# Optimization experiments

Hardware: AMD Instinct MI355X
Metric: run time of the kernel (lower is better)

## Reference

```python
import jax, jax.numpy as jnp
import numpy as np
from jax import lax


def setup_inputs() -> dict:
    key = jax.random.key(0)
    ks = jax.random.split(key, 5)
    B, Cin, H, W = 16, 256, 64, 64
    E, Cout, K = 8, 256, 3
    fan_in = Cin * K * K
    wscale = 1.0 / np.sqrt(fan_in)
    return {
        "x": jax.random.normal(ks[0], (B, Cin, H, W), dtype=jnp.float32),
        "weight": jax.random.normal(ks[1], (E, Cout, Cin, K, K), dtype=jnp.float32) * wscale,
        "bias": jax.random.normal(ks[2], (E, Cout), dtype=jnp.float32) * wscale,
        "routing_w": jax.random.normal(ks[3], (E, Cin), dtype=jnp.float32) * (1.0 / np.sqrt(Cin)),
        "routing_b": jnp.zeros((E,), dtype=jnp.float32),
    }


def reference(x, weight, bias, routing_w, routing_b):
    # Routing: global avg pool -> linear -> sigmoid  => [B, E]
    pooled = x.mean(axis=(2, 3))                                  # [B, Cin]
    routing = jax.nn.sigmoid(pooled @ routing_w.T + routing_b)    # [B, E]

    # Per-sample aggregated conv weights/bias (mixture of experts)
    agg_w = jnp.einsum('be,eoihw->boihw', routing, weight)        # [B, O, I, kh, kw]
    agg_b = routing @ bias                                        # [B, O]

    # Per-sample conv2d (stride=1, padding=1, dilation=1, groups=1), batched via vmap
    def conv_one(xi, wi):
        return lax.conv_general_dilated(
            xi[None], wi,
            window_strides=(1, 1),
            padding=((1, 1), (1, 1)),
            dimension_numbers=('NCHW', 'OIHW', 'NCHW'),
        )[0]

    out = jax.vmap(conv_one)(x, agg_w)                            # [B, O, H, W]
    return out + agg_b[:, :, None, None]
```

## Files before the change

### kernel.cpp

```cpp
#include <hip/hip_runtime.h>
#include <hip/hip_bf16.h>

typedef unsigned short u16;
typedef __attribute__((ext_vector_type(8))) short bf16x8;
typedef __attribute__((ext_vector_type(8))) short short8;
typedef __attribute__((ext_vector_type(4))) float f32x4;

#define B_ 16
#define CIN 256
#define COUT 256
#define NPIX 4096
#define E_ 8
#define HP 66
#define PPIX (HP*HP)
#define KTOT 2304
#define NKT 36

__device__ __forceinline__ u16 f2bf(float f){
    union { float f; unsigned int u; } v; v.f = f;
    return (u16)((v.u + 0x7FFFu + ((v.u >> 16) & 1u)) >> 16);
}

__device__ __forceinline__ void gload(const u16* g, u16* l){
    __builtin_amdgcn_global_load_lds(
        (const __attribute__((address_space(1))) unsigned int*)g,
        (__attribute__((address_space(3))) unsigned int*)l, 16, 0, 0);
}

__global__ void k_xt(const float* __restrict__ x, u16* __restrict__ xt2,
                     float* __restrict__ pooled){
    __shared__ float tile[64][65];
    int bid = blockIdx.x;
    int t = threadIdx.x;

    if (bid < 520){
        int gid = bid*256 + t;
        int u4 = gid & 31;
        int pl = gid >> 5;
        if (pl < B_*260){
            int bb = pl / 260;
            int pi = pl - bb*260;
            int yy, xx;
            if (pi < 66)      { yy = 0;  xx = pi; }
            else if (pi < 132){ yy = 65; xx = pi - 66; }
            else { int q = pi - 132; yy = 1 + (q >> 1); xx = (q & 1) ? 65 : 0; }
            uint4 z = {0u,0u,0u,0u};
            *(uint4*)(xt2 + ((size_t)bb*PPIX + yy*HP + xx)*CIN + u4*8) = z;
        }
    }

    int b = bid >> 8, ct = (bid >> 6) & 3, pt = bid & 63;
    int c0 = ct*64, p0 = pt*64;
    #pragma unroll
    for (int iter = 0; iter < 4; ++iter){
        int idx = t*4 + iter*1024;
        int r = idx >> 6, c4 = idx & 63;
        float4 v = *(const float4*)(x + ((size_t)(b*CIN + c0 + r))*NPIX + p0 + c4);
        tile[r][c4+0] = v.x; tile[r][c4+1] = v.y; tile[r][c4+2] = v.z; tile[r][c4+3] = v.w;
        float rs = v.x + v.y + v.z + v.w;
        #pragma unroll
        for (int off = 1; off < 16; off <<= 1) rs += __shfl_xor(rs, off, 64);
        if ((t & 15) == 0) atomicAdd(&pooled[b*CIN + c0 + r], rs);
    }
    __syncthreads();
    #pragma unroll
    for (int iter = 0; iter < 2; ++iter){
        int unit = t + iter*256;
        int g_l = unit & 7, pr = unit >> 3;
        unsigned int d0, d1, d2, d3;
        asm("v_cvt_pk_bf16_f32 %0, %1, %2" : "=v"(d0)
            : "v"(tile[g_l*8+0][pr]), "v"(tile[g_l*8+1][pr]));
        asm("v_cvt_pk_bf16_f32 %0, %1, %2" : "=v"(d1)
            : "v"(tile[g_l*8+2][pr]), "v"(tile[g_l*8+3][pr]));
        asm("v_cvt_pk_bf16_f32 %0, %1, %2" : "=v"(d2)
            : "v"(tile[g_l*8+4][pr]), "v"(tile[g_l*8+5][pr]));
        asm("v_cvt_pk_bf16_f32 %0, %1, %2" : "=v"(d3)
            : "v"(tile[g_l*8+6][pr]), "v"(tile[g_l*8+7][pr]));
        uint4 o; o.x = d0; o.y = d1; o.z = d2; o.w = d3;
        int p = p0 + pr;
        int yy = p >> 6, xx = p & 63;
        *(uint4*)(xt2 + ((size_t)b*PPIX + (yy+1)*HP + (xx+1))*CIN + c0 + g_l*8) = o;
    }
}

__global__ __launch_bounds__(576) void k_aggw(
    const float* __restrict__ weight, const float* __restrict__ pooled,
    const float* __restrict__ rw, const float* __restrict__ rb,
    const float* __restrict__ bias,
    u16* __restrict__ aggw, float* __restrict__ aggb)
{
    __shared__ float wls[E_][2304];
    __shared__ float r_s[B_*E_];
    int o = blockIdx.x, t = threadIdx.x;

    if (t < B_*E_){
        int b = t >> 3, e = t & 7;
        const float4* pp = (const float4*)(pooled + b*CIN);
        const float4* wp = (const float4*)(rw + e*CIN);
        float s = 0.f;
        #pragma unroll
        for (int i = 0; i < 64; ++i){
            float4 a = pp[i], c = wp[i];
            s += a.x*c.x + a.y*c.y + a.z*c.z + a.w*c.w;
        }
        s = s * (1.0f/(float)NPIX) + rb[e];
        r_s[t] = 1.0f/(1.0f + __expf(-s));
    }
    #pragma unroll
    for (int e = 0; e < E_; ++e){
        const float4* src = (const float4*)(weight + ((size_t)(e*COUT + o))*2304);
        float4* dst = (float4*)wls[e];
        dst[t] = src[t];
    }
    __syncthreads();

    if (t < B_){
        float s = 0.f;
        #pragma unroll
        for (int e = 0; e < E_; ++e) s += r_s[t*E_+e]*bias[e*COUT+o];
        aggb[t*COUT + o] = s;
    }

    {
        int grp = (t >= 288);
        int u = t - grp*288;
        int tp = u >> 5, cg = u & 31;
        float w[E_][8];
        #pragma unroll
        for (int e = 0; e < E_; ++e)
            #pragma unroll
            for (int j = 0; j < 8; ++j)
                w[e][j] = wls[e][(cg*8 + j)*9 + tp];

        int b0 = grp*8;
        for (int bb = 0; bb < 8; ++bb){
            int b = b0 + bb;
            float acc[8];
            #pragma unroll
            for (int j = 0; j < 8; ++j) acc[j] = 0.f;
            #pragma unroll
            for (int e = 0; e < E_; ++e){
                float r = r_s[b*E_ + e];
                #pragma unroll
                for (int j = 0; j < 8; ++j) acc[j] += r * w[e][j];
            }
            short8 ov;
            #pragma unroll
            for (int jj = 0; jj < 4; ++jj){
                unsigned int d;
                asm("v_cvt_pk_bf16_f32 %0, %1, %2" : "=v"(d) : "v"(acc[2*jj]), "v"(acc[2*jj+1]));
                ov[2*jj]   = (short)(d & 0xFFFF);
                ov[2*jj+1] = (short)(d >> 16);
            }
            *(short8*)(aggw + (((size_t)(b*COUT + o))*9 + tp)*CIN + cg*8) = ov;
        }
    }
}

__global__ __launch_bounds__(512, 2) void k_conv(
    const u16* __restrict__ aggw, const u16* __restrict__ xt2,
    const float* __restrict__ aggb, float* __restrict__ out)
{
    __shared__ __align__(16) u16 lds[65536];

    int orig = blockIdx.x;
    int bid = (orig & 7)*32 + (orig >> 3);

    int b  = bid >> 4;
    int nt = bid & 15;
    int y0 = nt << 2;

    int t = threadIdx.x;
    int lane = t & 63;
    int w = t >> 6;
    int wm = (w >> 2) << 7;
    int wn = (w & 3) << 6;
    int l16 = lane & 15;
    int kh4 = lane >> 4;
    int sw  = l16 & 7;

    int tr = t >> 3;
    int tc = t & 7;
    int sc = tc ^ (tr & 7);

    const u16* aSrc = aggw + (size_t)b*COUT*9*CIN + (size_t)tr*KTOT + sc*8;
    const u16* bSrc = xt2 + ((size_t)b*PPIX + (size_t)y0*HP + tr)*CIN + sc*8;

    f32x4 acc[8][4];
    #pragma unroll
    for (int i = 0; i < 8; ++i)
        #pragma unroll
        for (int j = 0; j < 4; ++j){
            f32x4 z = {0.f,0.f,0.f,0.f};
            acc[i][j] = z;
        }

    auto stage = [&](int kt, int bufn){
        int tap = kt >> 2;
        int c0  = (kt & 3) << 6;
        int kh  = tap / 3, kw = tap - kh*3;
        const u16* a0 = aSrc + tap*CIN + c0;
        const u16* b0 = bSrc + (kh*HP + kw)*CIN + c0;
        u16* dA = lds + bufn*32768 + w*512;
        u16* dB = dA + 16384;
        #pragma unroll
        for (int i = 0; i < 4; ++i)
            gload(a0 + (size_t)i*64*KTOT, dA + i*4096);
        #pragma unroll
        for (int i = 0; i < 4; ++i)
            gload(b0 + (size_t)i*HP*CIN, dB + i*4096);
    };

    int ck0 = ((kh4    ) ^ sw) * 8;
    int ck1 = ((kh4 | 4) ^ sw) * 8;

    stage(0, 0);
    __syncthreads();

    int buf = 0;
    #pragma unroll 2
    for (int kt = 0; kt < NKT; ++kt){
        const u16* LA = lds + buf*32768;
        const u16* LB = LA + 16384;

        bf16x8 af[2][4][2];
        bf16x8 bfr[2][2][2];

        #pragma unroll
        for (int mf = 0; mf < 4; ++mf){
            int ro = (wm + mf*16 + l16) * 64;
            af[0][mf][0] = *(const bf16x8*)(LA + ro + ck0);
            af[0][mf][1] = *(const bf16x8*)(LA + ro + ck1);
        }
        #pragma unroll
        for (int nf = 0; nf < 2; ++nf){
            int ro = (wn + nf*16 + l16) * 64;
            bfr[0][nf][0] = *(const bf16x8*)(LB + ro + ck0);
            bfr[0][nf][1] = *(const bf16x8*)(LB + ro + ck1);
        }

        if (kt < NKT-1) stage(kt+1, buf^1);

        #pragma unroll
        for (int nf = 0; nf < 2; ++nf){
            int ro = (wn + 32 + nf*16 + l16) * 64;
            bfr[1][nf][0] = *(const bf16x8*)(LB + ro + ck0);
            bfr[1][nf][1] = *(const bf16x8*)(LB + ro + ck1);
        }
        #pragma unroll
        for (int mf = 0; mf < 4; ++mf){
            int ro = (wm + 64 + mf*16 + l16) * 64;
            af[1][mf][0] = *(const bf16x8*)(LA + ro + ck0);
            af[1][mf][1] = *(const bf16x8*)(LA + ro + ck1);
        }

        #pragma unroll
        for (int qm = 0; qm < 2; ++qm)
            #pragma unroll
            for (int qn = 0; qn < 2; ++qn){
                #pragma unroll
                for (int mf = 0; mf < 4; ++mf)
                    #pragma unroll
                    for (int nf = 0; nf < 2; ++nf){
                        acc[qm*4+mf][qn*2+nf] = __builtin_amdgcn_mfma_f32_16x16x32_bf16(
                            af[qm][mf][0], bfr[qn][nf][0], acc[qm*4+mf][qn*2+nf], 0, 0, 0);
                        acc[qm*4+mf][qn*2+nf] = __builtin_amdgcn_mfma_f32_16x16x32_bf16(
                            af[qm][mf][1], bfr[qn][nf][1], acc[qm*4+mf][qn*2+nf], 0, 0, 0);
                    }
            }

        __syncthreads();
        buf ^= 1;
    }

    const float* ab = aggb + b*COUT;
    float* outp = out + ((size_t)b*COUT)*NPIX + nt*256;
    #pragma unroll
    for (int mf8 = 0; mf8 < 8; ++mf8){
        #pragma unroll
        for (int v = 0; v < 4; ++v){
            int r = wm + mf8*16 + (kh4 << 2) + v;
            float bias_r = ab[r];
            float* orow = outp + (size_t)r*NPIX;
            #pragma unroll
            for (int nf = 0; nf < 4; ++nf)
                orow[wn + nf*16 + l16] = acc[mf8][nf][v] + bias_r;
        }
    }
}

extern "C" void kernel_launch(void* const* d_in, const int* in_sizes, int n_in,
                              void* d_out, int out_size, void* d_ws, size_t ws_size,
                              hipStream_t stream)
{
    const float* x      = (const float*)d_in[0];
    const float* weight = (const float*)d_in[1];
    const float* bias   = (const float*)d_in[2];
    const float* rw     = (const float*)d_in[3];
    const float* rb     = (const float*)d_in[4];
    float* out = (float*)d_out;

    char* ws = (char*)d_ws;
    u16*   aggw    = (u16*)(ws);
    u16*   xt2     = (u16*)(ws + 18874368);
    float* pooled  = (float*)(ws + 54558720);
    float* aggb    = (float*)(ws + 54558720 + 16384);

    hipMemsetAsync(pooled, 0, B_*CIN*sizeof(float), stream);
    k_xt   <<<4096, 256, 0, stream>>>(x, xt2, pooled);
    k_aggw <<<COUT, 576, 0, stream>>>(weight, pooled, rw, rb, bias, aggw, aggb);
    k_conv <<<256,  512, 0, stream>>>(aggw, xt2, aggb, out);
}
```

Before: 113.3 us.

## Use BK=32 k-tiles with 4-buffer ring, processing two tiles per barrier

The conv GEMM main loop now splits K into 72 tiles of 32 instead of 36 tiles of 64. A four-slot LDS ring holds them, and two tiles are prefetched while the current pair is computed, so there is one barrier per two tiles and loads land two steps ahead. The LDS swizzle and staging addressing are reworked to match 32-wide rows, and launch bounds drop to one block per SM for more registers. The aim is deeper prefetch and fewer barriers, at the cost of lower occupancy and higher register pressure from holding two fragment sets.

```diff
diff --git a/kernel.cpp b/kernel.cpp
--- a/kernel.cpp
+++ b/kernel.cpp
@@ -14,7 +14,7 @@
 #define HP 66
 #define PPIX (HP*HP)
 #define KTOT 2304
-#define NKT 36
+#define NKT2 72
 
 __device__ __forceinline__ u16 f2bf(float f){
     union { float f; unsigned int u; } v; v.f = f;
@@ -157,7 +157,7 @@
     }
 }
 
-__global__ __launch_bounds__(512, 2) void k_conv(
+__global__ __launch_bounds__(512, 1) void k_conv(
     const u16* __restrict__ aggw, const u16* __restrict__ xt2,
     const float* __restrict__ aggb, float* __restrict__ out)
 {
@@ -177,14 +177,14 @@
     int wn = (w & 3) << 6;
     int l16 = lane & 15;
     int kh4 = lane >> 4;
-    int sw  = l16 & 7;
-
-    int tr = t >> 3;
-    int tc = t & 7;
-    int sc = tc ^ (tr & 7);
-
-    const u16* aSrc = aggw + (size_t)b*COUT*9*CIN + (size_t)tr*KTOT + sc*8;
-    const u16* bSrc = xt2 + ((size_t)b*PPIX + (size_t)y0*HP + tr)*CIN + sc*8;
+
+    int ck = ((kh4 ^ ((l16 >> 1) & 3)) << 3);
+
+    int sr  = t >> 2;
+    int lc8 = (((t & 3) ^ ((sr >> 1) & 3)) << 3);
+
+    const u16* aS = aggw + (size_t)b*COUT*9*CIN + (size_t)sr*(9*CIN) + lc8;
+    const u16* bS = xt2 + ((size_t)b*PPIX + (size_t)(y0 + (sr >> 6))*HP + (sr & 63))*CIN + lc8;
 
     f32x4 acc[8][4];
     #pragma unroll
@@ -196,81 +196,54 @@
         }
 
     auto stage = [&](int kt, int bufn){
-        int tap = kt >> 2;
-        int c0  = (kt & 3) << 6;
+        int tap = kt >> 3;
+        int c0  = (kt & 7) << 5;
         int kh  = tap / 3, kw = tap - kh*3;
-        const u16* a0 = aSrc + tap*CIN + c0;
-        const u16* b0 = bSrc + (kh*HP + kw)*CIN + c0;
-        u16* dA = lds + bufn*32768 + w*512;
-        u16* dB = dA + 16384;
-        #pragma unroll
-        for (int i = 0; i < 4; ++i)
-            gload(a0 + (size_t)i*64*KTOT, dA + i*4096);
-        #pragma unroll
-        for (int i = 0; i < 4; ++i)
-            gload(b0 + (size_t)i*HP*CIN, dB + i*4096);
+        const u16* a0 = aS + tap*CIN + c0;
+        const u16* b0 = bS + (kh*HP + kw)*CIN + c0;
+        u16* base = lds + bufn*16384 + w*512;
+        gload(a0, base);
+        gload(a0 + (size_t)128*9*CIN, base + 4096);
+        gload(b0, base + 8192);
+        gload(b0 + (size_t)2*HP*CIN, base + 12288);
     };
 
-    int ck0 = ((kh4    ) ^ sw) * 8;
-    int ck1 = ((kh4 | 4) ^ sw) * 8;
+    auto rd = [&](const u16* LA, bf16x8 (&af)[8], bf16x8 (&bv)[4]){
+        const u16* LB = LA + 8192;
+        #pragma unroll
+        for (int mf = 0; mf < 8; ++mf)
+            af[mf] = *(const bf16x8*)(LA + (wm + mf*16 + l16)*32 + ck);
+        #pragma unroll
+        for (int nf = 0; nf < 4; ++nf)
+            bv[nf] = *(const bf16x8*)(LB + (wn + nf*16 + l16)*32 + ck);
+    };
+    auto mma = [&](bf16x8 (&af)[8], bf16x8 (&bv)[4]){
+        #pragma unroll
+        for (int mf = 0; mf < 8; ++mf)
+            #pragma unroll
+            for (int nf = 0; nf < 4; ++nf)
+                acc[mf][nf] = __builtin_amdgcn_mfma_f32_16x16x32_bf16(
+                    af[mf], bv[nf], acc[mf][nf], 0, 0, 0);
+    };
 
     stage(0, 0);
+    stage(1, 1);
     __syncthreads();
 
-    int buf = 0;
-    #pragma unroll 2
-    for (int kt = 0; kt < NKT; ++kt){
-        const u16* LA = lds + buf*32768;
-        const u16* LB = LA + 16384;
-
-        bf16x8 af[2][4][2];
-        bf16x8 bfr[2][2][2];
-
-        #pragma unroll
-        for (int mf = 0; mf < 4; ++mf){
-            int ro = (wm + mf*16 + l16) * 64;
-            af[0][mf][0] = *(const bf16x8*)(LA + ro + ck0);
-            af[0][mf][1] = *(const bf16x8*)(LA + ro + ck1);
-        }
-        #pragma unroll
-        for (int nf = 0; nf < 2; ++nf){
-            int ro = (wn + nf*16 + l16) * 64;
-            bfr[0][nf][0] = *(const bf16x8*)(LB + ro + ck0);
-            bfr[0][nf][1] = *(const bf16x8*)(LB + ro + ck1);
-        }
-
-        if (kt < NKT-1) stage(kt+1, buf^1);
-
-        #pragma unroll
-        for (int nf = 0; nf < 2; ++nf){
-            int ro = (wn + 32 + nf*16 + l16) * 64;
-            bfr[1][nf][0] = *(const bf16x8*)(LB + ro + ck0);
-            bfr[1][nf][1] = *(const bf16x8*)(LB + ro + ck1);
-        }
-        #pragma unroll
-        for (int mf = 0; mf < 4; ++mf){
-            int ro = (wm + 64 + mf*16 + l16) * 64;
-            af[1][mf][0] = *(const bf16x8*)(LA + ro + ck0);
-            af[1][mf][1] = *(const bf16x8*)(LA + ro + ck1);
-        }
-
-        #pragma unroll
-        for (int qm = 0; qm < 2; ++qm)
-            #pragma unroll
-            for (int qn = 0; qn < 2; ++qn){
-                #pragma unroll
-                for (int mf = 0; mf < 4; ++mf)
-                    #pragma unroll
-                    for (int nf = 0; nf < 2; ++nf){
-                        acc[qm*4+mf][qn*2+nf] = __builtin_amdgcn_mfma_f32_16x16x32_bf16(
-                            af[qm][mf][0], bfr[qn][nf][0], acc[qm*4+mf][qn*2+nf], 0, 0, 0);
-                        acc[qm*4+mf][qn*2+nf] = __builtin_amdgcn_mfma_f32_16x16x32_bf16(
-                            af[qm][mf][1], bfr[qn][nf][1], acc[qm*4+mf][qn*2+nf], 0, 0, 0);
-                    }
-            }
+    for (int s = 0; s < NKT2; s += 2){
+        bf16x8 afA[8], bvA[4], afB[8], bvB[4];
+
+        rd(lds + (s & 3)*16384, afA, bvA);
+
+        if (s + 2 < NKT2) stage(s + 2, (s + 2) & 3);
+        if (s + 3 < NKT2) stage(s + 3, (s + 3) & 3);
+
+        rd(lds + ((s + 1) & 3)*16384, afB, bvB);
+
+        mma(afA, bvA);
+        mma(afB, bvB);
 
         __syncthreads();
-        buf ^= 1;
     }
 
     const float* ab = aggb + b*COUT;
```

Measured after the change: 120.5 us. 1.06x slower.
